# Performance work log

Hardware: AMD Instinct MI355X
Metric: run time of the kernel (lower is better)

The kernel has to match this reference:

```python
import math
import jax, jax.numpy as jnp
import numpy as np

V, D, L, H, B, T = 50257, 1024, 6, 16, 4, 1024
HD = D // H  # 64


def layer_norm(x, s, b, eps=1e-5):
    m = jnp.mean(x, axis=-1, keepdims=True)
    v = jnp.var(x, axis=-1, keepdims=True)
    return (x - m) * jax.lax.rsqrt(v + eps) * s + b


def setup_inputs() -> dict:
    key = jax.random.key(0)
    ks = jax.random.split(key, 8)
    sc = 0.02
    return {
        "input_ids": jax.random.randint(ks[0], (B, T), 0, V),
        "attention_mask": jnp.ones((B, T), jnp.float32),
        "pool_mask": jax.random.uniform(ks[1], (B, T), dtype=jnp.float32),
        "embed": jax.random.normal(ks[2], (V, D), jnp.float32) * sc,
        "ln1_s": jnp.ones((L, D), jnp.float32),
        "ln1_b": jnp.zeros((L, D), jnp.float32),
        "qkv_w": jax.random.normal(ks[3], (L, D, 3 * D), jnp.float32) * sc,
        "qkv_b": jnp.zeros((L, 3 * D), jnp.float32),
        "attn_w": jax.random.normal(ks[4], (L, D, D), jnp.float32) * sc,
        "attn_b": jnp.zeros((L, D), jnp.float32),
        "ln2_s": jnp.ones((L, D), jnp.float32),
        "ln2_b": jnp.zeros((L, D), jnp.float32),
        "fc1_w": jax.random.normal(ks[5], (L, D, 4 * D), jnp.float32) * sc,
        "fc1_b": jnp.zeros((L, 4 * D), jnp.float32),
        "fc2_w": jax.random.normal(ks[6], (L, 4 * D, D), jnp.float32) * sc,
        "fc2_b": jnp.zeros((L, D), jnp.float32),
    }


def reference(input_ids, attention_mask, pool_mask, embed, ln1_s, ln1_b,
              qkv_w, qkv_b, attn_w, attn_b, ln2_s, ln2_b,
              fc1_w, fc1_b, fc2_w, fc2_b):
    h = embed[input_ids]  # [B,T,D]
    # key_mask.clamp(min=0) then log(clamp(min=1e-9)) == log(clip(mask, 1e-9))
    log_mask = jnp.log(jnp.clip(attention_mask, 1e-9))[:, None, None, :]  # [B,1,1,T]
    scale = 1.0 / math.sqrt(HD)

    def block(h, p):
        l1s, l1b, qw, qb, aw, ab, l2s, l2b, f1w, f1b, f2w, f2b = p
        x = layer_norm(h, l1s, l1b)
        qkv = jnp.einsum('btd,de->bte', x, qw) + qb          # [B,T,3D]
        qkv = qkv.reshape(B, T, H, 3 * HD).transpose(0, 2, 1, 3)  # [B,H,T,3hd]
        q, k, v = jnp.split(qkv, 3, axis=-1)
        scores = jnp.einsum('bhqd,bhkd->bhqk', q, k) * scale + log_mask
        probs = jax.nn.softmax(scores, axis=-1)
        ctx = jnp.einsum('bhqk,bhkd->bhqd', probs, v)
        ctx = ctx.transpose(0, 2, 1, 3).reshape(B, T, D)
        h = h + jnp.einsum('btd,de->bte', ctx, aw) + ab
        y = layer_norm(h, l2s, l2b)
        y = jax.nn.gelu(jnp.einsum('btd,df->btf', y, f1w) + f1b, approximate=False)
        h = h + jnp.einsum('btf,fd->btd', y, f2w) + f2b
        # NOTE: source applies post_attention_layernorm a second time at block end
        h = layer_norm(h, l2s, l2b)
        return h, None

    params = (ln1_s, ln1_b, qkv_w, qkv_b, attn_w, attn_b,
              ln2_s, ln2_b, fc1_w, fc1_b, fc2_w, fc2_b)
    h, _ = jax.lax.scan(block, h, params)

    # pool with pool_mask, then L2-normalize (F.normalize, eps=1e-12)
    m = pool_mask[..., None]
    sent = (h * m).sum(axis=1) / jnp.clip(m.sum(axis=1), 1e-6)
    return sent / jnp.clip(jnp.linalg.norm(sent, axis=-1, keepdims=True), 1e-12)
```

## Files before the change

kernel.cpp:

```cpp
#include <hip/hip_runtime.h>
#include <hip/hip_bf16.h>
#include <math.h>

#define VV 50257
#define DD 1024
#define LL 6
#define HH 16
#define BB 4
#define TT 1024
#define HD 64
#define BT (BB*TT)

typedef __attribute__((ext_vector_type(8))) short bf16x8;
typedef __attribute__((ext_vector_type(8))) _Float16 f16x8;
typedef __attribute__((ext_vector_type(4))) float f32x4;
typedef __attribute__((ext_vector_type(16))) float f32x16;

__device__ inline float b2f(unsigned short u) {
    unsigned x = ((unsigned)u) << 16;
    return __uint_as_float(x);
}
__device__ inline unsigned short f2b(float f) {
    __hip_bfloat16 h = __float2bfloat16(f);
    return *reinterpret_cast<unsigned short*>(&h);
}
__device__ inline void plswap32(unsigned &dst, unsigned &src) {
    asm("v_permlane32_swap_b32 %0, %1" : "+v"(dst), "+v"(src));
}

#define GLOAD16(g, l) __builtin_amdgcn_global_load_lds( \
    (const __attribute__((address_space(1))) void*)(g), \
    (__attribute__((address_space(3))) void*)(l), 16, 0, 0)

__launch_bounds__(256)
__global__ void gather_embed(const int* __restrict__ ids, const float* __restrict__ emb,
                             float* __restrict__ h) {
    const int row = blockIdx.x;
    const int id = ids[row];
    const float4* src = (const float4*)(emb + (size_t)id * DD);
    float4* dst = (float4*)(h + (size_t)row * DD);
    dst[threadIdx.x] = src[threadIdx.x];
}

__launch_bounds__(256)
__global__ void logmask_k(const float* __restrict__ am, float* __restrict__ lm) {
    int i = blockIdx.x * 256 + threadIdx.x;
    if (i < BT) lm[i] = logf(fmaxf(am[i], 1e-9f));
}

__device__ inline float block_sum_256(float v, float* ws) {
    #pragma unroll
    for (int o = 32; o > 0; o >>= 1) v += __shfl_down(v, o);
    const int lane = threadIdx.x & 63, wid = threadIdx.x >> 6;
    if (lane == 0) ws[wid] = v;
    __syncthreads();
    return ws[0] + ws[1] + ws[2] + ws[3];
}

__launch_bounds__(256)
__global__ void ln_f32(const float* __restrict__ in, float* __restrict__ out,
                       const float* __restrict__ g, const float* __restrict__ bta) {
    __shared__ float ws1[4], ws2[4];
    const int row = blockIdx.x, tid = threadIdx.x;
    const float* x = in + (size_t)row * DD;
    float4 v = *(const float4*)(x + tid * 4);
    float s = v.x + v.y + v.z + v.w;
    float tot = block_sum_256(s, ws1);
    float m = tot * (1.0f / 1024.0f);
    float d0 = v.x - m, d1 = v.y - m, d2 = v.z - m, d3 = v.w - m;
    float s2 = d0*d0 + d1*d1 + d2*d2 + d3*d3;
    float tot2 = block_sum_256(s2, ws2);
    float rstd = rsqrtf(tot2 * (1.0f / 1024.0f) + 1e-5f);
    const int d = tid * 4;
    float4 gg = *(const float4*)(g + d);
    float4 bb = *(const float4*)(bta + d);
    float4 o;
    o.x = d0 * rstd * gg.x + bb.x;
    o.y = d1 * rstd * gg.y + bb.y;
    o.z = d2 * rstd * gg.z + bb.z;
    o.w = d3 * rstd * gg.w + bb.w;
    *(float4*)(out + (size_t)row * DD + d) = o;
}

__launch_bounds__(256)
__global__ void ln_bf16(const float* __restrict__ in, unsigned short* __restrict__ out,
                        const float* __restrict__ g, const float* __restrict__ bta) {
    __shared__ float ws1[4], ws2[4];
    const int row = blockIdx.x, tid = threadIdx.x;
    const float* x = in + (size_t)row * DD;
    float4 v = *(const float4*)(x + tid * 4);
    float s = v.x + v.y + v.z + v.w;
    float tot = block_sum_256(s, ws1);
    float m = tot * (1.0f / 1024.0f);
    float d0 = v.x - m, d1 = v.y - m, d2 = v.z - m, d3 = v.w - m;
    float s2 = d0*d0 + d1*d1 + d2*d2 + d3*d3;
    float tot2 = block_sum_256(s2, ws2);
    float rstd = rsqrtf(tot2 * (1.0f / 1024.0f) + 1e-5f);
    const int d = tid * 4;
    float4 gg = *(const float4*)(g + d);
    float4 bb = *(const float4*)(bta + d);
    ushort4 o;
    o.x = f2b(d0 * rstd * gg.x + bb.x);
    o.y = f2b(d1 * rstd * gg.y + bb.y);
    o.z = f2b(d2 * rstd * gg.z + bb.z);
    o.w = f2b(d3 * rstd * gg.w + bb.w);
    *(ushort4*)(out + (size_t)row * DD + d) = o;
}

__launch_bounds__(256)
__global__ void ln_dual(const float* __restrict__ in, float* __restrict__ outf,
                        const float* __restrict__ g2, const float* __restrict__ b2v,
                        unsigned short* __restrict__ outb,
                        const float* __restrict__ g1, const float* __restrict__ b1v) {
    __shared__ float ws1[4], ws2[4], ws3[4], ws4[4];
    const int row = blockIdx.x, tid = threadIdx.x;
    const int d = tid * 4;
    float4 v = *(const float4*)(in + (size_t)row * DD + d);
    float s = v.x + v.y + v.z + v.w;
    float m = block_sum_256(s, ws1) * (1.0f / 1024.0f);
    float d0 = v.x - m, d1 = v.y - m, d2 = v.z - m, d3 = v.w - m;
    float s2 = d0*d0 + d1*d1 + d2*d2 + d3*d3;
    float rstd = rsqrtf(block_sum_256(s2, ws2) * (1.0f / 1024.0f) + 1e-5f);
    float4 gg = *(const float4*)(g2 + d);
    float4 bb = *(const float4*)(b2v + d);
    float4 y;
    y.x = d0 * rstd * gg.x + bb.x;
    y.y = d1 * rstd * gg.y + bb.y;
    y.z = d2 * rstd * gg.z + bb.z;
    y.w = d3 * rstd * gg.w + bb.w;
    *(float4*)(outf + (size_t)row * DD + d) = y;
    float t = y.x + y.y + y.z + y.w;
    float m2 = block_sum_256(t, ws3) * (1.0f / 1024.0f);
    float e0 = y.x - m2, e1 = y.y - m2, e2 = y.z - m2, e3 = y.w - m2;
    float t2 = e0*e0 + e1*e1 + e2*e2 + e3*e3;
    float rstd2 = rsqrtf(block_sum_256(t2, ws4) * (1.0f / 1024.0f) + 1e-5f);
    float4 g1v = *(const float4*)(g1 + d);
    float4 b1x = *(const float4*)(b1v + d);
    ushort4 o;
    o.x = f2b(e0 * rstd2 * g1v.x + b1x.x);
    o.y = f2b(e1 * rstd2 * g1v.y + b1x.y);
    o.z = f2b(e2 * rstd2 * g1v.z + b1x.z);
    o.w = f2b(e3 * rstd2 * g1v.w + b1x.w);
    *(ushort4*)(outb + (size_t)row * DD + d) = o;
}

__launch_bounds__(256)
__global__ void wtrans4(const float* __restrict__ wq, unsigned short* __restrict__ wqo,
                        const float* __restrict__ wa, unsigned short* __restrict__ wao,
                        const float* __restrict__ w1, unsigned short* __restrict__ w1o,
                        const float* __restrict__ w2, unsigned short* __restrict__ w2o) {
    __shared__ float tile[64][65];
    int id = blockIdx.x;
    const float* W; unsigned short* Wt; int K, N, tx, ty;
    if (id < 768)       { W = wq; Wt = wqo; K = 1024; N = 3072; tx = id % 48; ty = id / 48; }
    else if (id < 1024) { id -= 768;  W = wa; Wt = wao; K = 1024; N = 1024; tx = id & 15; ty = id >> 4; }
    else if (id < 2048) { id -= 1024; W = w1; Wt = w1o; K = 1024; N = 4096; tx = id & 63; ty = id >> 6; }
    else                { id -= 2048; W = w2; Wt = w2o; K = 4096; N = 1024; tx = id & 15; ty = id >> 4; }
    const int k0 = ty * 64, n0 = tx * 64;
    const int lrow = threadIdx.x >> 4;
    const int lcol = (threadIdx.x & 15) * 4;
    #pragma unroll
    for (int i = 0; i < 4; ++i) {
        const int r = lrow + i * 16;
        *(float4*)&tile[r][lcol] = *(const float4*)(W + (size_t)(k0 + r) * N + n0 + lcol);
    }
    __syncthreads();
    #pragma unroll
    for (int i = 0; i < 4; ++i) {
        const int n = lrow + i * 16;
        ushort4 o;
        o.x = f2b(tile[lcol + 0][n]);
        o.y = f2b(tile[lcol + 1][n]);
        o.z = f2b(tile[lcol + 2][n]);
        o.w = f2b(tile[lcol + 3][n]);
        *(ushort4*)(Wt + (size_t)(n0 + n) * K + k0 + lcol) = o;
    }
}

#define BM 128
#define BK 64

__device__ inline float gelu_f(float v) {
    return 0.5f * v * (1.0f + erff(v * 0.70710678118654752f));
}

template<int EPI, int NFRAG>
__launch_bounds__(256)
__global__ void gemm_mfma(const unsigned short* __restrict__ A,
                          const unsigned short* __restrict__ Bt,
                          const float* __restrict__ bias, void* __restrict__ Cv,
                          int M, int K, int N) {
    constexpr int BN = NFRAG * 32;
    __shared__ short As[BM * BK];
    __shared__ short Bs[BN * BK];

    const int tid = threadIdx.x;
    const int wid = tid >> 6, lane = tid & 63;

    const int nwg = gridDim.x * gridDim.y;
    int bid = blockIdx.y * gridDim.x + blockIdx.x;
    bid = (bid & 7) * (nwg >> 3) + (bid >> 3);
    const int m0 = (bid / gridDim.x) * BM;
    const int n0 = (bid % gridDim.x) * BN;

    const int wr = wid >> 1, wc = wid & 1;
    const int fr = lane & 15, fq = lane >> 4;

    const int rowS = tid >> 3;
    const int cS = tid & 7;
    const int coff = (cS ^ (rowS & 7)) * 8;
    const unsigned short* aS = A  + (size_t)(m0 + rowS) * K + coff;
    const unsigned short* bS = Bt + (size_t)(n0 + rowS) * K + coff;
    const size_t rstride = (size_t)32 * K;

    const int key = fr & 7;
    const int c0 = fq ^ key;
    int aoff[4], boff[NFRAG];
    #pragma unroll
    for (int m = 0; m < 4; ++m) aoff[m] = (wr * 64 + m * 16 + fr) * BK + c0 * 8;
    #pragma unroll
    for (int n = 0; n < NFRAG; ++n) boff[n] = (wc * (NFRAG * 16) + n * 16 + fr) * BK + c0 * 8;

    f32x4 acc[4][NFRAG];
    #pragma unroll
    for (int m = 0; m < 4; ++m)
        #pragma unroll
        for (int n = 0; n < NFRAG; ++n) acc[m][n] = (f32x4){0.f, 0.f, 0.f, 0.f};

    for (int kk = 0; kk < K; kk += BK) {
        __syncthreads();
        #pragma unroll
        for (int r = 0; r < 4; ++r)
            GLOAD16(aS + kk + r * rstride, &As[(wid * 64 + r * 256) * 8]);
        #pragma unroll
        for (int r = 0; r < NFRAG; ++r)
            GLOAD16(bS + kk + r * rstride, &Bs[(wid * 64 + r * 256) * 8]);
        __syncthreads();
        #pragma unroll
        for (int s = 0; s < 2; ++s) {
            bf16x8 af[4], bfr[NFRAG];
            #pragma unroll
            for (int m = 0; m < 4; ++m) af[m] = *(const bf16x8*)&As[aoff[m] ^ (s << 5)];
            #pragma unroll
            for (int n = 0; n < NFRAG; ++n) bfr[n] = *(const bf16x8*)&Bs[boff[n] ^ (s << 5)];
            #pragma unroll
            for (int m = 0; m < 4; ++m)
                #pragma unroll
                for (int n = 0; n < NFRAG; ++n)
                    acc[m][n] = __builtin_amdgcn_mfma_f32_16x16x32_bf16(
                        af[m], bfr[n], acc[m][n], 0, 0, 0);
        }
    }

    float bias_v[NFRAG];
    #pragma unroll
    for (int n = 0; n < NFRAG; ++n) bias_v[n] = bias[n0 + wc * (NFRAG * 16) + n * 16 + fr];

    #pragma unroll
    for (int m = 0; m < 4; ++m) {
        #pragma unroll
        for (int n = 0; n < NFRAG; ++n) {
            const int col = n0 + wc * (NFRAG * 16) + n * 16 + fr;
            #pragma unroll
            for (int j = 0; j < 4; ++j) {
                const int row = m0 + wr * 64 + m * 16 + fq * 4 + j;
                float v = acc[m][n][j] + bias_v[n];
                if (EPI == 1) {
                    float* C = (float*)Cv;
                    C[(size_t)row * N + col] += v;
                } else {
                    if (EPI == 2) v = gelu_f(v);
                    unsigned short* C = (unsigned short*)Cv;
                    C[(size_t)row * N + col] = f2b(v);
                }
            }
        }
    }
}

__launch_bounds__(256)
__global__ void attn_mfma(const unsigned short* __restrict__ qkv,
                          const float* __restrict__ lm,
                          unsigned short* __restrict__ ctx) {
    int bid = blockIdx.x;
    const int ww = (bid & 7) * 64 + (bid >> 3);
    const int bh = ww >> 3, qt = ww & 7;
    const int b = bh >> 4, hh = bh & 15;
    const int tid = threadIdx.x, w = tid >> 6, lane = tid & 63;
    const int lo = lane & 31, hf = lane >> 5;
    const int q_row = qt * 128 + w * 32 + lo;

    __shared__ short Ks[2][64 * 64];
    __shared__ short Vt[2][64 * 72];
    __shared__ float lms[2][64];

    bf16x8 qf[4];
    {
        const unsigned short* qbase = qkv + (size_t)(b * TT + q_row) * 3072 + hh * 192;
        #pragma unroll
        for (int kk = 0; kk < 4; ++kk)
            qf[kk] = *(const bf16x8*)(qbase + (2 * kk + hf) * 8);
    }

    const int r0 = tid >> 3, cS = tid & 7;
    const unsigned short* kp = qkv + (size_t)(b * TT + r0) * 3072 + hh * 192 + 64
                               + ((cS ^ (r0 & 7)) * 8);
    const int vkey = tid & 31, vc = tid >> 5;
    const unsigned short* vp = qkv + (size_t)(b * TT + vkey) * 3072 + hh * 192 + 128 + vc * 8;
    const float* lmrow = lm + b * TT;

    f32x16 o0, o1;
    #pragma unroll
    for (int j = 0; j < 16; ++j) { o0[j] = 0.f; o1[j] = 0.f; }
    float M = -1e30f, S = 0.f;

    {
        GLOAD16(kp, &Ks[0][(w * 64) * 8]);
        GLOAD16(kp + (size_t)32 * 3072, &Ks[0][(256 + w * 64) * 8]);
        bf16x8 v0 = *(const bf16x8*)vp;
        bf16x8 v1 = *(const bf16x8*)(vp + (size_t)32 * 3072);
        if (tid < 64) lms[0][tid] = lmrow[tid];
        #pragma unroll
        for (int i = 0; i < 8; ++i) {
            _Float16 h0 = (_Float16)b2f((unsigned short)v0[i]);
            _Float16 h1 = (_Float16)b2f((unsigned short)v1[i]);
            Vt[0][(vc * 8 + i) * 72 + vkey] = *reinterpret_cast<short*>(&h0);
            Vt[0][(vc * 8 + i) * 72 + 32 + vkey] = *reinterpret_cast<short*>(&h1);
        }
    }

    int cur = 0;
    for (int kt = 0; kt < 16; ++kt) {
        __syncthreads();
        if (kt < 15) {
            const int nb = cur ^ 1;
            const size_t off = (size_t)((kt + 1) * 64) * 3072;
            GLOAD16(kp + off, &Ks[nb][(w * 64) * 8]);
            GLOAD16(kp + off + (size_t)32 * 3072, &Ks[nb][(256 + w * 64) * 8]);
            bf16x8 v0 = *(const bf16x8*)(vp + off);
            bf16x8 v1 = *(const bf16x8*)(vp + off + (size_t)32 * 3072);
            if (tid < 64) lms[nb][tid] = lmrow[(kt + 1) * 64 + tid];
            #pragma unroll
            for (int i = 0; i < 8; ++i) {
                _Float16 h0 = (_Float16)b2f((unsigned short)v0[i]);
                _Float16 h1 = (_Float16)b2f((unsigned short)v1[i]);
                Vt[nb][(vc * 8 + i) * 72 + vkey] = *reinterpret_cast<short*>(&h0);
                Vt[nb][(vc * 8 + i) * 72 + 32 + vkey] = *reinterpret_cast<short*>(&h1);
            }
        }

        #pragma unroll
        for (int g = 0; g < 2; ++g) {
            f32x16 s16;
            #pragma unroll
            for (int j = 0; j < 16; ++j) s16[j] = 0.f;
            __builtin_amdgcn_s_setprio(1);
            #pragma unroll
            for (int kk = 0; kk < 4; ++kk) {
                const int c = (2 * kk + hf) ^ (lo & 7);
                bf16x8 kf = *(const bf16x8*)&Ks[cur][((g * 32 + lo) * 8 + c) * 8];
                s16 = __builtin_amdgcn_mfma_f32_32x32x16_bf16(kf, qf[kk], s16, 0, 0, 0);
            }
            __builtin_amdgcn_s_setprio(0);

            float p[16];
            float mx = -1e30f;
            #pragma unroll
            for (int j = 0; j < 16; ++j) {
                const int kidx = g * 32 + (j & 3) + 8 * (j >> 2) + 4 * hf;
                float sv = s16[j] * 0.125f + lms[cur][kidx];
                p[j] = sv;
                mx = fmaxf(mx, sv);
            }
            mx = fmaxf(mx, __shfl_xor(mx, 32));
            if (!__all(mx <= M + 8.0f)) {
                const float Mn = fmaxf(M, mx);
                const float f = __expf(M - Mn);
                S *= f;
                #pragma unroll
                for (int j = 0; j < 16; ++j) { o0[j] *= f; o1[j] *= f; }
                M = Mn;
            }

            unsigned short ph[16];
            float ls = 0.f;
            #pragma unroll
            for (int j = 0; j < 16; ++j) {
                _Float16 hq = (_Float16)__expf(p[j] - M);
                ph[j] = *reinterpret_cast<unsigned short*>(&hq);
                ls += (float)hq;
            }
            ls += __shfl_xor(ls, 32);
            S += ls;

            unsigned ra = (unsigned)ph[0]  | ((unsigned)ph[1]  << 16);
            unsigned rb = (unsigned)ph[2]  | ((unsigned)ph[3]  << 16);
            unsigned rc = (unsigned)ph[4]  | ((unsigned)ph[5]  << 16);
            unsigned rd = (unsigned)ph[6]  | ((unsigned)ph[7]  << 16);
            unsigned re = (unsigned)ph[8]  | ((unsigned)ph[9]  << 16);
            unsigned rf = (unsigned)ph[10] | ((unsigned)ph[11] << 16);
            unsigned rg = (unsigned)ph[12] | ((unsigned)ph[13] << 16);
            unsigned rh = (unsigned)ph[14] | ((unsigned)ph[15] << 16);
            plswap32(ra, rc);
            plswap32(rb, rd);
            plswap32(re, rg);
            plswap32(rf, rh);
            union { unsigned u[4]; f16x8 v; } p1, p2;
            p1.u[0] = ra; p1.u[1] = rb; p1.u[2] = rc; p1.u[3] = rd;
            p2.u[0] = re; p2.u[1] = rf; p2.u[2] = rg; p2.u[3] = rh;

            f16x8 va0 = *(const f16x8*)&Vt[cur][lo * 72 + g * 32 + hf * 8];
            f16x8 va1 = *(const f16x8*)&Vt[cur][lo * 72 + g * 32 + 16 + hf * 8];
            f16x8 vb0 = *(const f16x8*)&Vt[cur][(32 + lo) * 72 + g * 32 + hf * 8];
            f16x8 vb1 = *(const f16x8*)&Vt[cur][(32 + lo) * 72 + g * 32 + 16 + hf * 8];
            __builtin_amdgcn_s_setprio(1);
            o0 = __builtin_amdgcn_mfma_f32_32x32x16_f16(va0, p1.v, o0, 0, 0, 0);
            o0 = __builtin_amdgcn_mfma_f32_32x32x16_f16(va1, p2.v, o0, 0, 0, 0);
            o1 = __builtin_amdgcn_mfma_f32_32x32x16_f16(vb0, p1.v, o1, 0, 0, 0);
            o1 = __builtin_amdgcn_mfma_f32_32x32x16_f16(vb1, p2.v, o1, 0, 0, 0);
            __builtin_amdgcn_s_setprio(0);
        }
        cur ^= 1;
    }

    const float inv = 1.f / S;
    unsigned short* obase = ctx + (size_t)(b * TT + q_row) * DD + hh * 64;
    #pragma unroll
    for (int g = 0; g < 4; ++g) {
        const int dbase = 8 * g + 4 * hf;
        ushort4 w0, w1;
        w0.x = f2b(o0[4*g+0] * inv); w0.y = f2b(o0[4*g+1] * inv);
        w0.z = f2b(o0[4*g+2] * inv); w0.w = f2b(o0[4*g+3] * inv);
        w1.x = f2b(o1[4*g+0] * inv); w1.y = f2b(o1[4*g+1] * inv);
        w1.z = f2b(o1[4*g+2] * inv); w1.w = f2b(o1[4*g+3] * inv);
        *(ushort4*)(obase + dbase) = w0;
        *(ushort4*)(obase + 32 + dbase) = w1;
    }
}

__launch_bounds__(256)
__global__ void pool_partial(const float* __restrict__ h, const float* __restrict__ pm,
                             float* __restrict__ part) {
    const int b = blockIdx.x >> 4, c = blockIdx.x & 15;
    const int tid = threadIdx.x;
    const float* hp = h + (size_t)(b * TT + c * 64) * DD + tid * 4;
    const float* pp = pm + b * TT + c * 64;
    float4 acc = {0.f, 0.f, 0.f, 0.f};
    for (int t = 0; t < 64; ++t) {
        const float p = pp[t];
        float4 v = *(const float4*)(hp + (size_t)t * DD);
        acc.x += p * v.x; acc.y += p * v.y; acc.z += p * v.z; acc.w += p * v.w;
    }
    *(float4*)(part + (size_t)blockIdx.x * DD + tid * 4) = acc;
}

__launch_bounds__(1024)
__global__ void pool_final(const float* __restrict__ part, const float* __restrict__ pm,
                           float* __restrict__ out) {
    const int b = blockIdx.x, d = threadIdx.x;
    __shared__ float ws[16];
    float s = pm[b * TT + d];
    #pragma unroll
    for (int o = 32; o > 0; o >>= 1) s += __shfl_down(s, o);
    if ((d & 63) == 0) ws[d >> 6] = s;
    __syncthreads();
    float msum = 0.f;
    #pragma unroll
    for (int i = 0; i < 16; ++i) msum += ws[i];

    float acc = 0.f;
    #pragma unroll
    for (int c = 0; c < 16; ++c)
        acc += part[(size_t)(b * 16 + c) * DD + d];
    const float sent = acc / fmaxf(msum, 1e-6f);

    float qv = sent * sent;
    #pragma unroll
    for (int o = 32; o > 0; o >>= 1) qv += __shfl_down(qv, o);
    __syncthreads();
    if ((d & 63) == 0) ws[d >> 6] = qv;
    __syncthreads();
    float nrm = 0.f;
    #pragma unroll
    for (int i = 0; i < 16; ++i) nrm += ws[i];
    nrm = sqrtf(nrm);
    out[b * DD + d] = sent / fmaxf(nrm, 1e-12f);
}

extern "C" void kernel_launch(void* const* d_in, const int* in_sizes, int n_in,
                              void* d_out, int out_size, void* d_ws, size_t ws_size,
                              hipStream_t stream) {
    const int*   ids    = (const int*)  d_in[0];
    const float* amask  = (const float*)d_in[1];
    const float* pmask  = (const float*)d_in[2];
    const float* embed  = (const float*)d_in[3];
    const float* ln1_s  = (const float*)d_in[4];
    const float* ln1_b  = (const float*)d_in[5];
    const float* qkv_w  = (const float*)d_in[6];
    const float* qkv_b  = (const float*)d_in[7];
    const float* attn_w = (const float*)d_in[8];
    const float* attn_b = (const float*)d_in[9];
    const float* ln2_s  = (const float*)d_in[10];
    const float* ln2_b  = (const float*)d_in[11];
    const float* fc1_w  = (const float*)d_in[12];
    const float* fc1_b  = (const float*)d_in[13];
    const float* fc2_w  = (const float*)d_in[14];
    const float* fc2_b  = (const float*)d_in[15];

    char* wp = (char*)d_ws;
    float* h = (float*)wp;                 wp += (size_t)BT * DD * 4;
    unsigned short* qkv_bf = (unsigned short*)wp; wp += (size_t)BT * 3072 * 2;
    unsigned short* act_bf = (unsigned short*)wp; wp += (size_t)BT * 4096 * 2;
    unsigned short* x_bf   = (unsigned short*)wp; wp += (size_t)BT * DD * 2;
    unsigned short* wq_t   = (unsigned short*)wp; wp += (size_t)3072 * 1024 * 2;
    unsigned short* wa_t   = (unsigned short*)wp; wp += (size_t)1024 * 1024 * 2;
    unsigned short* w1_t   = (unsigned short*)wp; wp += (size_t)4096 * 1024 * 2;
    unsigned short* w2_t   = (unsigned short*)wp; wp += (size_t)1024 * 4096 * 2;
    float* lm = (float*)wp;                wp += (size_t)BT * 4;
    float* part = (float*)wp;              wp += (size_t)64 * DD * 4;

    gather_embed<<<BT, 256, 0, stream>>>(ids, embed, h);
    logmask_k<<<16, 256, 0, stream>>>(amask, lm);
    ln_bf16<<<BT, 256, 0, stream>>>(h, x_bf, ln1_s, ln1_b);

    for (int l = 0; l < LL; ++l) {
        const size_t lD = (size_t)l * DD;

        wtrans4<<<3072, 256, 0, stream>>>(
            qkv_w + (size_t)l * 1024 * 3072, wq_t,
            attn_w + (size_t)l * 1024 * 1024, wa_t,
            fc1_w + (size_t)l * 1024 * 4096, w1_t,
            fc2_w + (size_t)l * 4096 * 1024, w2_t);

        gemm_mfma<0, 4><<<dim3(3072/128, BT/BM), 256, 0, stream>>>(
            x_bf, wq_t, qkv_b + (size_t)l * 3072, qkv_bf, BT, 1024, 3072);
        attn_mfma<<<512, 256, 0, stream>>>(qkv_bf, lm, x_bf);
        gemm_mfma<1, 2><<<dim3(1024/64, BT/BM), 256, 0, stream>>>(
            x_bf, wa_t, attn_b + lD, h, BT, 1024, 1024);
        ln_bf16<<<BT, 256, 0, stream>>>(h, x_bf, ln2_s + lD, ln2_b + lD);
        gemm_mfma<2, 4><<<dim3(4096/128, BT/BM), 256, 0, stream>>>(
            x_bf, w1_t, fc1_b + (size_t)l * 4096, act_bf, BT, 1024, 4096);
        gemm_mfma<1, 2><<<dim3(1024/64, BT/BM), 256, 0, stream>>>(
            act_bf, w2_t, fc2_b + lD, h, BT, 4096, 1024);

        if (l < LL - 1) {
            ln_dual<<<BT, 256, 0, stream>>>(h, h, ln2_s + lD, ln2_b + lD,
                                            x_bf, ln1_s + lD + DD, ln1_b + lD + DD);
        } else {
            ln_f32<<<BT, 256, 0, stream>>>(h, h, ln2_s + lD, ln2_b + lD);
        }
    }

    pool_partial<<<64, 256, 0, stream>>>(h, pmask, part);
    pool_final<<<BB, 1024, 0, stream>>>(part, pmask, (float*)d_out);
}
```

Before: 1.630 ms.

## Switch GEMMs to 32x32x16 MFMA, batch weight transposes, fuse gather with LN

```diff
diff --git a/kernel.cpp b/kernel.cpp
--- a/kernel.cpp
+++ b/kernel.cpp
@@ -32,22 +32,6 @@
     (const __attribute__((address_space(1))) void*)(g), \
     (__attribute__((address_space(3))) void*)(l), 16, 0, 0)
 
-__launch_bounds__(256)
-__global__ void gather_embed(const int* __restrict__ ids, const float* __restrict__ emb,
-                             float* __restrict__ h) {
-    const int row = blockIdx.x;
-    const int id = ids[row];
-    const float4* src = (const float4*)(emb + (size_t)id * DD);
-    float4* dst = (float4*)(h + (size_t)row * DD);
-    dst[threadIdx.x] = src[threadIdx.x];
-}
-
-__launch_bounds__(256)
-__global__ void logmask_k(const float* __restrict__ am, float* __restrict__ lm) {
-    int i = blockIdx.x * 256 + threadIdx.x;
-    if (i < BT) lm[i] = logf(fmaxf(am[i], 1e-9f));
-}
-
 __device__ inline float block_sum_256(float v, float* ws) {
     #pragma unroll
     for (int o = 32; o > 0; o >>= 1) v += __shfl_down(v, o);
@@ -55,6 +39,37 @@
     if (lane == 0) ws[wid] = v;
     __syncthreads();
     return ws[0] + ws[1] + ws[2] + ws[3];
+}
+
+__launch_bounds__(256)
+__global__ void gather_ln(const int* __restrict__ ids, const float* __restrict__ emb,
+                          float* __restrict__ h, unsigned short* __restrict__ xb,
+                          const float* __restrict__ g, const float* __restrict__ bta) {
+    __shared__ float ws1[4], ws2[4];
+    const int row = blockIdx.x, tid = threadIdx.x;
+    const int id = ids[row];
+    const int d = tid * 4;
+    float4 v = *(const float4*)(emb + (size_t)id * DD + d);
+    *(float4*)(h + (size_t)row * DD + d) = v;
+    float s = v.x + v.y + v.z + v.w;
+    float m = block_sum_256(s, ws1) * (1.0f / 1024.0f);
+    float d0 = v.x - m, d1 = v.y - m, d2 = v.z - m, d3 = v.w - m;
+    float s2 = d0*d0 + d1*d1 + d2*d2 + d3*d3;
+    float rstd = rsqrtf(block_sum_256(s2, ws2) * (1.0f / 1024.0f) + 1e-5f);
+    float4 gg = *(const float4*)(g + d);
+    float4 bb = *(const float4*)(bta + d);
+    ushort4 o;
+    o.x = f2b(d0 * rstd * gg.x + bb.x);
+    o.y = f2b(d1 * rstd * gg.y + bb.y);
+    o.z = f2b(d2 * rstd * gg.z + bb.z);
+    o.w = f2b(d3 * rstd * gg.w + bb.w);
+    *(ushort4*)(xb + (size_t)row * DD + d) = o;
+}
+
+__launch_bounds__(256)
+__global__ void logmask_k(const float* __restrict__ am, float* __restrict__ lm) {
+    int i = blockIdx.x * 256 + threadIdx.x;
+    if (i < BT) lm[i] = logf(fmaxf(am[i], 1e-9f));
 }
 
 __launch_bounds__(256)
@@ -65,12 +80,10 @@
     const float* x = in + (size_t)row * DD;
     float4 v = *(const float4*)(x + tid * 4);
     float s = v.x + v.y + v.z + v.w;
-    float tot = block_sum_256(s, ws1);
-    float m = tot * (1.0f / 1024.0f);
+    float m = block_sum_256(s, ws1) * (1.0f / 1024.0f);
     float d0 = v.x - m, d1 = v.y - m, d2 = v.z - m, d3 = v.w - m;
     float s2 = d0*d0 + d1*d1 + d2*d2 + d3*d3;
-    float tot2 = block_sum_256(s2, ws2);
-    float rstd = rsqrtf(tot2 * (1.0f / 1024.0f) + 1e-5f);
+    float rstd = rsqrtf(block_sum_256(s2, ws2) * (1.0f / 1024.0f) + 1e-5f);
     const int d = tid * 4;
     float4 gg = *(const float4*)(g + d);
     float4 bb = *(const float4*)(bta + d);
@@ -90,12 +103,10 @@
     const float* x = in + (size_t)row * DD;
     float4 v = *(const float4*)(x + tid * 4);
     float s = v.x + v.y + v.z + v.w;
-    float tot = block_sum_256(s, ws1);
-    float m = tot * (1.0f / 1024.0f);
+    float m = block_sum_256(s, ws1) * (1.0f / 1024.0f);
     float d0 = v.x - m, d1 = v.y - m, d2 = v.z - m, d3 = v.w - m;
     float s2 = d0*d0 + d1*d1 + d2*d2 + d3*d3;
-    float tot2 = block_sum_256(s2, ws2);
-    float rstd = rsqrtf(tot2 * (1.0f / 1024.0f) + 1e-5f);
+    float rstd = rsqrtf(block_sum_256(s2, ws2) * (1.0f / 1024.0f) + 1e-5f);
     const int d = tid * 4;
     float4 gg = *(const float4*)(g + d);
     float4 bb = *(const float4*)(bta + d);
@@ -145,17 +156,18 @@
 }
 
 __launch_bounds__(256)
-__global__ void wtrans4(const float* __restrict__ wq, unsigned short* __restrict__ wqo,
-                        const float* __restrict__ wa, unsigned short* __restrict__ wao,
-                        const float* __restrict__ w1, unsigned short* __restrict__ w1o,
-                        const float* __restrict__ w2, unsigned short* __restrict__ w2o) {
+__global__ void wtrans_all(const float* __restrict__ wq, unsigned short* __restrict__ wqo,
+                           const float* __restrict__ wa, unsigned short* __restrict__ wao,
+                           const float* __restrict__ w1, unsigned short* __restrict__ w1o,
+                           const float* __restrict__ w2, unsigned short* __restrict__ w2o) {
     __shared__ float tile[64][65];
-    int id = blockIdx.x;
+    const int l = blockIdx.x / 3072;
+    int id = blockIdx.x % 3072;
     const float* W; unsigned short* Wt; int K, N, tx, ty;
-    if (id < 768)       { W = wq; Wt = wqo; K = 1024; N = 3072; tx = id % 48; ty = id / 48; }
-    else if (id < 1024) { id -= 768;  W = wa; Wt = wao; K = 1024; N = 1024; tx = id & 15; ty = id >> 4; }
-    else if (id < 2048) { id -= 1024; W = w1; Wt = w1o; K = 1024; N = 4096; tx = id & 63; ty = id >> 6; }
-    else                { id -= 2048; W = w2; Wt = w2o; K = 4096; N = 1024; tx = id & 15; ty = id >> 4; }
+    if (id < 768)       { W = wq + (size_t)l*1024*3072; Wt = wqo + (size_t)l*3072*1024; K = 1024; N = 3072; tx = id % 48; ty = id / 48; }
+    else if (id < 1024) { id -= 768;  W = wa + (size_t)l*1024*1024; Wt = wao + (size_t)l*1024*1024; K = 1024; N = 1024; tx = id & 15; ty = id >> 4; }
+    else if (id < 2048) { id -= 1024; W = w1 + (size_t)l*1024*4096; Wt = w1o + (size_t)l*4096*1024; K = 1024; N = 4096; tx = id & 63; ty = id >> 6; }
+    else                { id -= 2048; W = w2 + (size_t)l*4096*1024; Wt = w2o + (size_t)l*1024*4096; K = 4096; N = 1024; tx = id & 15; ty = id >> 4; }
     const int k0 = ty * 64, n0 = tx * 64;
     const int lrow = threadIdx.x >> 4;
     const int lcol = (threadIdx.x & 15) * 4;
@@ -184,18 +196,19 @@
     return 0.5f * v * (1.0f + erff(v * 0.70710678118654752f));
 }
 
-template<int EPI, int NFRAG>
+template<int EPI, int NF32>
 __launch_bounds__(256)
 __global__ void gemm_mfma(const unsigned short* __restrict__ A,
                           const unsigned short* __restrict__ Bt,
                           const float* __restrict__ bias, void* __restrict__ Cv,
                           int M, int K, int N) {
-    constexpr int BN = NFRAG * 32;
+    constexpr int BN = NF32 * 64;
     __shared__ short As[BM * BK];
     __shared__ short Bs[BN * BK];
 
     const int tid = threadIdx.x;
     const int wid = tid >> 6, lane = tid & 63;
+    const int lo = lane & 31, hf = lane >> 5;
 
     const int nwg = gridDim.x * gridDim.y;
     int bid = blockIdx.y * gridDim.x + blockIdx.x;
@@ -204,28 +217,29 @@
     const int n0 = (bid % gridDim.x) * BN;
 
     const int wr = wid >> 1, wc = wid & 1;
-    const int fr = lane & 15, fq = lane >> 4;
-
-    const int rowS = tid >> 3;
-    const int cS = tid & 7;
+
+    const int rowS = tid >> 3, cS = tid & 7;
     const int coff = (cS ^ (rowS & 7)) * 8;
     const unsigned short* aS = A  + (size_t)(m0 + rowS) * K + coff;
     const unsigned short* bS = Bt + (size_t)(n0 + rowS) * K + coff;
     const size_t rstride = (size_t)32 * K;
 
-    const int key = fr & 7;
-    const int c0 = fq ^ key;
-    int aoff[4], boff[NFRAG];
-    #pragma unroll
-    for (int m = 0; m < 4; ++m) aoff[m] = (wr * 64 + m * 16 + fr) * BK + c0 * 8;
-    #pragma unroll
-    for (int n = 0; n < NFRAG; ++n) boff[n] = (wc * (NFRAG * 16) + n * 16 + fr) * BK + c0 * 8;
-
-    f32x4 acc[4][NFRAG];
-    #pragma unroll
-    for (int m = 0; m < 4; ++m)
-        #pragma unroll
-        for (int n = 0; n < NFRAG; ++n) acc[m][n] = (f32x4){0.f, 0.f, 0.f, 0.f};
+    int cph[4];
+    #pragma unroll
+    for (int ks = 0; ks < 4; ++ks) cph[ks] = ((ks * 2 + hf) ^ (lo & 7)) * 8;
+    int arow[2], brow[NF32];
+    #pragma unroll
+    for (int m = 0; m < 2; ++m) arow[m] = (wr * 64 + m * 32 + lo) * BK;
+    #pragma unroll
+    for (int n = 0; n < NF32; ++n) brow[n] = (wc * NF32 * 32 + n * 32 + lo) * BK;
+
+    f32x16 acc[2][NF32];
+    #pragma unroll
+    for (int m = 0; m < 2; ++m)
+        #pragma unroll
+        for (int n = 0; n < NF32; ++n)
+            #pragma unroll
+            for (int j = 0; j < 16; ++j) acc[m][n][j] = 0.f;
 
     for (int kk = 0; kk < K; kk += BK) {
         __syncthreads();
@@ -233,38 +247,36 @@
         for (int r = 0; r < 4; ++r)
             GLOAD16(aS + kk + r * rstride, &As[(wid * 64 + r * 256) * 8]);
         #pragma unroll
-        for (int r = 0; r < NFRAG; ++r)
+        for (int r = 0; r < 2 * NF32; ++r)
             GLOAD16(bS + kk + r * rstride, &Bs[(wid * 64 + r * 256) * 8]);
         __syncthreads();
         #pragma unroll
-        for (int s = 0; s < 2; ++s) {
-            bf16x8 af[4], bfr[NFRAG];
-            #pragma unroll
-            for (int m = 0; m < 4; ++m) af[m] = *(const bf16x8*)&As[aoff[m] ^ (s << 5)];
-            #pragma unroll
-            for (int n = 0; n < NFRAG; ++n) bfr[n] = *(const bf16x8*)&Bs[boff[n] ^ (s << 5)];
-            #pragma unroll
-            for (int m = 0; m < 4; ++m)
+        for (int ks = 0; ks < 4; ++ks) {
+            bf16x8 af[2], bfr[NF32];
+            #pragma unroll
+            for (int m = 0; m < 2; ++m) af[m] = *(const bf16x8*)&As[arow[m] + cph[ks]];
+            #pragma unroll
+            for (int n = 0; n < NF32; ++n) bfr[n] = *(const bf16x8*)&Bs[brow[n] + cph[ks]];
+            #pragma unroll
+            for (int m = 0; m < 2; ++m)
                 #pragma unroll
-                for (int n = 0; n < NFRAG; ++n)
-                    acc[m][n] = __builtin_amdgcn_mfma_f32_16x16x32_bf16(
+                for (int n = 0; n < NF32; ++n)
+                    acc[m][n] = __builtin_amdgcn_mfma_f32_32x32x16_bf16(
                         af[m], bfr[n], acc[m][n], 0, 0, 0);
         }
     }
 
-    float bias_v[NFRAG];
-    #pragma unroll
-    for (int n = 0; n < NFRAG; ++n) bias_v[n] = bias[n0 + wc * (NFRAG * 16) + n * 16 + fr];
-
-    #pragma unroll
-    for (int m = 0; m < 4; ++m) {
-        #pragma unroll
-        for (int n = 0; n < NFRAG; ++n) {
-            const int col = n0 + wc * (NFRAG * 16) + n * 16 + fr;
-            #pragma unroll
-            for (int j = 0; j < 4; ++j) {
-                const int row = m0 + wr * 64 + m * 16 + fq * 4 + j;
-                float v = acc[m][n][j] + bias_v[n];
+    #pragma unroll
+    for (int n = 0; n < NF32; ++n) {
+        const int col = n0 + wc * NF32 * 32 + n * 32 + lo;
+        const float bias_v = bias[col];
+        #pragma unroll
+        for (int m = 0; m < 2; ++m) {
+            const int rbase = m0 + wr * 64 + m * 32 + 4 * hf;
+            #pragma unroll
+            for (int j = 0; j < 16; ++j) {
+                const int row = rbase + (j & 3) + 8 * (j >> 2);
+                float v = acc[m][n][j] + bias_v;
                 if (EPI == 1) {
                     float* C = (float*)Cv;
                     C[(size_t)row * N + col] += v;
@@ -512,36 +524,35 @@
     unsigned short* qkv_bf = (unsigned short*)wp; wp += (size_t)BT * 3072 * 2;
     unsigned short* act_bf = (unsigned short*)wp; wp += (size_t)BT * 4096 * 2;
     unsigned short* x_bf   = (unsigned short*)wp; wp += (size_t)BT * DD * 2;
-    unsigned short* wq_t   = (unsigned short*)wp; wp += (size_t)3072 * 1024 * 2;
-    unsigned short* wa_t   = (unsigned short*)wp; wp += (size_t)1024 * 1024 * 2;
-    unsigned short* w1_t   = (unsigned short*)wp; wp += (size_t)4096 * 1024 * 2;
-    unsigned short* w2_t   = (unsigned short*)wp; wp += (size_t)1024 * 4096 * 2;
+    unsigned short* wq_t   = (unsigned short*)wp; wp += (size_t)LL * 3072 * 1024 * 2;
+    unsigned short* wa_t   = (unsigned short*)wp; wp += (size_t)LL * 1024 * 1024 * 2;
+    unsigned short* w1_t   = (unsigned short*)wp; wp += (size_t)LL * 4096 * 1024 * 2;
+    unsigned short* w2_t   = (unsigned short*)wp; wp += (size_t)LL * 1024 * 4096 * 2;
     float* lm = (float*)wp;                wp += (size_t)BT * 4;
     float* part = (float*)wp;              wp += (size_t)64 * DD * 4;
 
-    gather_embed<<<BT, 256, 0, stream>>>(ids, embed, h);
+    gather_ln<<<BT, 256, 0, stream>>>(ids, embed, h, x_bf, ln1_s, ln1_b);
     logmask_k<<<16, 256, 0, stream>>>(amask, lm);
-    ln_bf16<<<BT, 256, 0, stream>>>(h, x_bf, ln1_s, ln1_b);
+    wtrans_all<<<LL * 3072, 256, 0, stream>>>(qkv_w, wq_t, attn_w, wa_t,
+                                              fc1_w, w1_t, fc2_w, w2_t);
 
     for (int l = 0; l < LL; ++l) {
         const size_t lD = (size_t)l * DD;
-
-        wtrans4<<<3072, 256, 0, stream>>>(
-            qkv_w + (size_t)l * 1024 * 3072, wq_t,
-            attn_w + (size_t)l * 1024 * 1024, wa_t,
-            fc1_w + (size_t)l * 1024 * 4096, w1_t,
-            fc2_w + (size_t)l * 4096 * 1024, w2_t);
-
-        gemm_mfma<0, 4><<<dim3(3072/128, BT/BM), 256, 0, stream>>>(
-            x_bf, wq_t, qkv_b + (size_t)l * 3072, qkv_bf, BT, 1024, 3072);
+        const unsigned short* wq = wq_t + (size_t)l * 3072 * 1024;
+        const unsigned short* wa = wa_t + (size_t)l * 1024 * 1024;
+        const unsigned short* w1 = w1_t + (size_t)l * 4096 * 1024;
+        const unsigned short* w2 = w2_t + (size_t)l * 1024 * 4096;
+
+        gemm_mfma<0, 2><<<dim3(3072/128, BT/BM), 256, 0, stream>>>(
+            x_bf, wq, qkv_b + (size_t)l * 3072, qkv_bf, BT, 1024, 3072);
         attn_mfma<<<512, 256, 0, stream>>>(qkv_bf, lm, x_bf);
-        gemm_mfma<1, 2><<<dim3(1024/64, BT/BM), 256, 0, stream>>>(
-            x_bf, wa_t, attn_b + lD, h, BT, 1024, 1024);
+        gemm_mfma<1, 1><<<dim3(1024/64, BT/BM), 256, 0, stream>>>(
+            x_bf, wa, attn_b + lD, h, BT, 1024, 1024);
         ln_bf16<<<BT, 256, 0, stream>>>(h, x_bf, ln2_s + lD, ln2_b + lD);
-        gemm_mfma<2, 4><<<dim3(4096/128, BT/BM), 256, 0, stream>>>(
-            x_bf, w1_t, fc1_b + (size_t)l * 4096, act_bf, BT, 1024, 4096);
-        gemm_mfma<1, 2><<<dim3(1024/64, BT/BM), 256, 0, stream>>>(
-            act_bf, w2_t, fc2_b + lD, h, BT, 4096, 1024);
+        gemm_mfma<2, 2><<<dim3(4096/128, BT/BM), 256, 0, stream>>>(
+            x_bf, w1, fc1_b + (size_t)l * 4096, act_bf, BT, 1024, 4096);
+        gemm_mfma<1, 1><<<dim3(1024/64, BT/BM), 256, 0, stream>>>(
+            act_bf, w2, fc2_b + lD, h, BT, 4096, 1024);
 
         if (l < LL - 1) {
             ln_dual<<<BT, 256, 0, stream>>>(h, h, ln2_s + lD, ln2_b + lD,
```

New measurement: 1.808 ms. +10.9%, slower.
